# Kernel optimization log

Measured on AMD Instinct MI355X. Metric: run time of the kernel, lower is better.

Reference implementation:

```python
import jax, jax.numpy as jnp
import numpy as np

DIM = 128
HEADS = 4
HEAD_DIM = DIM // HEADS
WIN = 7
DIL = 1
EPS = 1e-5
HIDDEN = 4 * DIM  # mlp_ratio = 4.0
PAD = DIL * (WIN // 2)


def setup_inputs() -> dict:
    key = jax.random.key(0)
    ks = jax.random.split(key, 16)
    s = 0.02
    return {
        "x": jax.random.normal(ks[0], (8, DIM, 256, 256), dtype=jnp.float32),
        "n1_w": jnp.ones((DIM,), jnp.float32),
        "n1_b": jnp.zeros((DIM,), jnp.float32),
        "qkv_w": jax.random.normal(ks[1], (3 * DIM, DIM), jnp.float32) * s,
        "qkv_b": jnp.zeros((3 * DIM,), jnp.float32),
        "proj_w": jax.random.normal(ks[2], (DIM, DIM), jnp.float32) * s,
        "proj_b": jnp.zeros((DIM,), jnp.float32),
        "n2_w": jnp.ones((DIM,), jnp.float32),
        "n2_b": jnp.zeros((DIM,), jnp.float32),
        "mlp_w1": jax.random.normal(ks[3], (HIDDEN, DIM), jnp.float32) * s,
        "mlp_b1": jnp.zeros((HIDDEN,), jnp.float32),
        "mlp_w2": jax.random.normal(ks[4], (DIM, HIDDEN), jnp.float32) * s,
        "mlp_b2": jnp.zeros((DIM,), jnp.float32),
    }


def _channel_ln(x, w, b):
    # LayerNorm over channel axis (axis=1) of NCHW, per spatial location
    mu = jnp.mean(x, axis=1, keepdims=True)
    var = jnp.mean(jnp.square(x - mu), axis=1, keepdims=True)
    xn = (x - mu) * jax.lax.rsqrt(var + EPS)
    return xn * w[None, :, None, None] + b[None, :, None, None]


def _local_attn(x, qkv_w, qkv_b, proj_w, proj_b):
    B, C, H, W = x.shape
    qkv = jnp.einsum("oc,bchw->bohw", qkv_w, x) + qkv_b[None, :, None, None]
    q, k, v = jnp.split(qkv, 3, axis=1)
    q = q.reshape(B, HEADS, HEAD_DIM, H, W) * (HEAD_DIM ** -0.5)
    k = k.reshape(B, HEADS, HEAD_DIM, H, W)
    v = v.reshape(B, HEADS, HEAD_DIM, H, W)
    # boundary_pad='zeros': pad key/value maps with zeros
    pad = [(0, 0), (0, 0), (0, 0), (PAD, PAD), (PAD, PAD)]
    kp = jnp.pad(k, pad)
    vp = jnp.pad(v, pad)
    offsets = [(oi, oj) for oi in range(WIN) for oj in range(WIN)]
    scores = []
    for oi, oj in offsets:  # fixed small window loop (49 iters)
        ks = kp[..., oi * DIL : oi * DIL + H, oj * DIL : oj * DIL + W]
        scores.append(jnp.einsum("bhcij,bhcij->bhij", q, ks))
    scores = jnp.stack(scores, axis=-1)
    attn = jax.nn.softmax(scores, axis=-1)
    out = jnp.zeros_like(v)
    for idx, (oi, oj) in enumerate(offsets):
        vs = vp[..., oi * DIL : oi * DIL + H, oj * DIL : oj * DIL + W]
        out = out + attn[..., idx][:, :, None] * vs
    out = out.reshape(B, C, H, W)
    return jnp.einsum("oc,bchw->bohw", proj_w, out) + proj_b[None, :, None, None]


def _mlp(x, w1, b1, w2, b2):
    h = jnp.einsum("oc,bchw->bohw", w1, x) + b1[None, :, None, None]
    h = jax.nn.gelu(h)
    return jnp.einsum("oc,bchw->bohw", w2, h) + b2[None, :, None, None]


def reference(x, n1_w, n1_b, qkv_w, qkv_b, proj_w, proj_b, n2_w, n2_b, mlp_w1, mlp_b1, mlp_w2, mlp_b2):
    x = x + _local_attn(_channel_ln(x, n1_w, n1_b), qkv_w, qkv_b, proj_w, proj_b)
    x = x + _mlp(_channel_ln(x, n2_w, n2_b), mlp_w1, mlp_b1, mlp_w2, mlp_b2)
    return x
```

## Files before the change

### kernel.cpp

```cpp
#include <hip/hip_runtime.h>
#include <hip/hip_bf16.h>

typedef unsigned short u16;
typedef unsigned int u32;
typedef __attribute__((ext_vector_type(4))) u32 u32x4;
typedef __attribute__((ext_vector_type(2))) u32 u32x2;
typedef __attribute__((ext_vector_type(8))) __bf16 bf16x8;
typedef __attribute__((ext_vector_type(4))) float f32x4;
typedef __attribute__((ext_vector_type(4))) short short4v;

#define HW 65536

__device__ __forceinline__ u16 f2bf(float f){
  union { u32 i; float f; } v; v.f = f;
  u32 r = v.i + 0x7fffu + ((v.i >> 16) & 1u);
  return (u16)(r >> 16);
}
__device__ __forceinline__ u32 pkbf(float a, float b){
  __bf16 lo = (__bf16)a, hi = (__bf16)b;
  u16 ulo = __builtin_bit_cast(u16, lo);
  u16 uhi = __builtin_bit_cast(u16, hi);
  return (u32)ulo | ((u32)uhi << 16);
}
__device__ __forceinline__ float rcpf(float x){
#if __has_builtin(__builtin_amdgcn_rcpf)
  return __builtin_amdgcn_rcpf(x);
#else
  return 1.0f / x;
#endif
}
__device__ __forceinline__ float gelu_tanh(float v){
  float t = v * v;
  float u = fmaf(0.044715f * t, v, v);
  float z = 1.5957691216057308f * u;
  float e = __expf(-z);
  return v * rcpf(1.0f + e);
}

__device__ __forceinline__ f32x4 mfma16bf16(short4v a, short4v b, f32x4 c){
#if __has_builtin(__builtin_amdgcn_mfma_f32_16x16x16bf16_1k)
  return __builtin_amdgcn_mfma_f32_16x16x16bf16_1k(a, b, c, 0, 0, 0);
#else
  f32x4 d;
  asm volatile("v_mfma_f32_16x16x16_bf16 %0, %1, %2, %3"
               : "=v"(d) : "v"(a), "v"(b), "v"(c));
  return d;
#endif
}

__global__ __launch_bounds__(256) void k_pack(
    const float* __restrict__ qkvw, const float* __restrict__ projw,
    const float* __restrict__ w1, const float* __restrict__ w2,
    u16* __restrict__ wf)
{
  int tile = blockIdx.x;
  int t = threadIdx.x;
  int l = t >> 1, half = t & 1;
  if (l >= 64) return;
  int lg = l >> 4;
  if (tile >= 256){
    int ti = tile - 256;
    int hp = ti >> 3, m = ti & 7;
    int row = m * 16 + (l & 15);
    u16 o[4];
    #pragma unroll
    for (int j = 0; j < 4; ++j){
      int s = half * 4 + j;
      int kloc = (s < 4) ? (4 * lg + s) : (16 + 4 * lg + (s - 4));
      o[j] = f2bf(w2[(size_t)row * 512 + hp * 32 + kloc]);
    }
    u32x2 v; v[0] = (u32)o[0] | ((u32)o[1] << 16); v[1] = (u32)o[2] | ((u32)o[3] << 16);
    *(u32x2*)(wf + 131072 + ti * 512 + l * 8 + half * 4) = v;
    return;
  }
  const float* W; int base, ti;
  if (tile < 96)       { W = qkvw; base = 0;     ti = tile; }
  else if (tile < 128) { W = projw; base = 49152; ti = tile - 96; }
  else                 { W = w1;   base = 65536; ti = tile - 128; }
  int mt = ti / 4, kt = ti % 4;
  int r0 = half * 4;
  int m = mt * 16 + (l & 15);
  int kb = kt * 32 + 8 * lg + r0;
  u16 o[4];
  #pragma unroll
  for (int j = 0; j < 4; ++j) o[j] = f2bf(W[(size_t)m * 128 + kb + j]);
  u32x2 v; v[0] = (u32)o[0] | ((u32)o[1] << 16); v[1] = (u32)o[2] | ((u32)o[3] << 16);
  *(u32x2*)(wf + base + ti * 512 + l * 8 + r0) = v;
}

__global__ __launch_bounds__(256, 2) void k_ln_qkv(
    const float* __restrict__ x, const float* __restrict__ n1w,
    const float* __restrict__ n1b, const u16* __restrict__ wfq,
    const float* __restrict__ qkvb, u16* __restrict__ qkvp)
{
  __shared__ __align__(16) char smem[66560];
  float* red  = (float*)(smem + 16384);
  float* mu_s = (float*)(smem + 18432);
  float* rs_s = (float*)(smem + 18688);

  const int t = threadIdx.x;
  const int w = t >> 6, l = t & 63;
  const int P0 = blockIdx.x * 64;
  const int b = P0 >> 16;
  const int pix0 = P0 & 65535;
  const float* xb = x + ((size_t)b * 128) * HW + pix0 + l;

  float xv[32];
  float s = 0.f, s2 = 0.f;
  #pragma unroll
  for (int j = 0; j < 32; ++j){
    float v = xb[(size_t)(w * 32 + j) * HW];
    xv[j] = v; s += v; s2 += v * v;
  }
  red[w * 64 + l] = s;
  red[256 + w * 64 + l] = s2;
  __syncthreads();
  if (t < 64){
    float ss  = red[t] + red[64 + t] + red[128 + t] + red[192 + t];
    float ss2 = red[256 + t] + red[320 + t] + red[384 + t] + red[448 + t];
    float mu = ss * 0.0078125f;
    float var = ss2 * 0.0078125f - mu * mu;
    mu_s[t] = mu; rs_s[t] = rsqrtf(var + 1e-5f);
  }
  __syncthreads();
  {
    float mu = mu_s[l], rs = rs_s[l];
    #pragma unroll
    for (int jj = 0; jj < 4; ++jj){
      int c0 = w * 32 + jj * 8;
      u32x4 pk;
      #pragma unroll
      for (int k2 = 0; k2 < 4; ++k2){
        float v0 = (xv[jj*8 + k2*2    ] - mu) * rs * n1w[c0 + k2*2    ] + n1b[c0 + k2*2    ];
        float v1 = (xv[jj*8 + k2*2 + 1] - mu) * rs * n1w[c0 + k2*2 + 1] + n1b[c0 + k2*2 + 1];
        pk[k2] = pkbf(v0, v1);
      }
      *(u32x4*)(smem + l * 256 + (((w * 4 + jj) ^ (l & 7)) << 4)) = pk;
    }
  }
  __syncthreads();

  const int lg = l >> 4, ln = l & 15;
  const bf16x8* wfrag = (const bf16x8*)wfq;
  f32x4 acc[6][4];
  #pragma unroll
  for (int m = 0; m < 6; ++m)
    #pragma unroll
    for (int n = 0; n < 4; ++n) acc[m][n] = (f32x4)(0.f);
  #pragma unroll
  for (int kt = 0; kt < 4; ++kt){
    bf16x8 a[6], bb[4];
    #pragma unroll
    for (int m = 0; m < 6; ++m) a[m] = wfrag[((w*6 + m)*4 + kt)*64 + l];
    #pragma unroll
    for (int n = 0; n < 4; ++n){
      int p = n * 16 + ln;
      bb[n] = *(const bf16x8*)(smem + p * 256 + ((((kt*4 + lg)) ^ (p & 7)) << 4));
    }
    #pragma unroll
    for (int m = 0; m < 6; ++m)
      #pragma unroll
      for (int n = 0; n < 4; ++n)
        acc[m][n] = __builtin_amdgcn_mfma_f32_16x16x32_bf16(a[m], bb[n], acc[m][n], 0, 0, 0);
  }
  #pragma unroll
  for (int m = 0; m < 6; ++m)
    #pragma unroll
    for (int n = 0; n < 4; ++n){
      int o0 = w * 96 + m * 16 + 4 * lg;
      float qs = (o0 < 128) ? 0.17677669529663687f : 1.0f;
      int p = n * 16 + ln;
      u32x2 v;
      v[0] = pkbf((acc[m][n][0] + qkvb[o0+0]) * qs, (acc[m][n][1] + qkvb[o0+1]) * qs);
      v[1] = pkbf((acc[m][n][2] + qkvb[o0+2]) * qs, (acc[m][n][3] + qkvb[o0+3]) * qs);
      *(u32x2*)(smem + 16384 + p * 784 + o0 * 2) = v;
    }
  __syncthreads();
  for (int i = t; i < 3072; i += 256){
    int p = i / 48, c8 = i - p * 48;
    u32x4 v = *(const u32x4*)(smem + 16384 + p * 784 + c8 * 16);
    int sel = c8 >> 4, hh = (c8 >> 2) & 3, c0 = (c8 & 3) * 8;
    u16* plane = qkvp + (size_t)sel * 67108864ull;
    *(u32x4*)(plane + (((size_t)(b*4 + hh)) * 65536 + pix0 + p) * 32 + c0) = v;
  }
}

__global__ __launch_bounds__(256, 2) void k_attn(
    u16* qbuf, const u16* __restrict__ kbuf, const u16* __restrict__ vbuf)
{
  __shared__ __align__(16) u16 Klds[4 * 512 * 8];
  __shared__ __align__(16) u16 VT[32 * 532 + 16];
  const int t = threadIdx.x;
  const int blk = blockIdx.x;
  const int tx16 = blk & 15, ty16 = (blk >> 4) & 15;
  const int h = (blk >> 8) & 3, b = blk >> 10;
  const int y0 = ty16 * 16, x0 = tx16 * 16;
  const int bh = b * 4 + h;
  const u16* kg = kbuf + (size_t)bh * 65536 * 32;
  const u16* vg = vbuf + (size_t)bh * 65536 * 32;

  for (int i = t; i < 2130; i += 256) ((u32x4*)VT)[i] = (u32x4){0u,0u,0u,0u};
  __syncthreads();

  for (int pix = t; pix < 484; pix += 256){
    int yy = pix / 22, xx = pix - yy * 22;
    int gy = y0 + yy - 3, gx = x0 + xx - 3;
    bool ok = (gy >= 0 && gy < 256 && gx >= 0 && gx < 256);
    u32x4 kv[4], vv[4];
    #pragma unroll
    for (int j = 0; j < 4; ++j){ kv[j] = (u32x4){0u,0u,0u,0u}; vv[j] = (u32x4){0u,0u,0u,0u}; }
    if (ok){
      size_t gb = ((size_t)(gy * 256 + gx)) * 32;
      #pragma unroll
      for (int j = 0; j < 4; ++j){
        kv[j] = *(const u32x4*)(kg + gb + j * 8);
        vv[j] = *(const u32x4*)(vg + gb + j * 8);
      }
    }
    #pragma unroll
    for (int j = 0; j < 4; ++j)
      *(u32x4*)(Klds + (j * 512 + pix) * 8) = kv[j];
    int vb = yy * 24 + xx;
    #pragma unroll
    for (int j = 0; j < 4; ++j)
      #pragma unroll
      for (int ww = 0; ww < 4; ++ww){
        int c = j * 8 + ww * 2;
        VT[(c    ) * 532 + vb] = (u16)(vv[j][ww] & 0xffffu);
        VT[(c + 1) * 532 + vb] = (u16)(vv[j][ww] >> 16);
      }
  }
  __syncthreads();

  const int l = t & 63, w = t >> 6;
  const int ln = l & 15, g = l >> 4;

  bool mk[2][4];
  #pragma unroll
  for (int sl = 0; sl < 2; ++sl)
    #pragma unroll
    for (int r = 0; r < 4; ++r)
      mk[sl][r] = ((unsigned)(sl * 16 + g * 4 + r - ln)) <= 6u;

  for (int rt = 0; rt < 4; ++rt){
    int yl = rt * 4 + w;
    int qpix = (y0 + yl) * 256 + x0 + ln;
    u16* qp = qbuf + ((size_t)bh * 65536 + qpix) * 32;
    bf16x8 qf = *(const bf16x8*)(qp + g * 8);

    f32x4 S[7][2];
    #pragma unroll
    for (int oi = 0; oi < 7; ++oi){
      int rowb = (yl + oi) * 22;
      #pragma unroll
      for (int sl = 0; sl < 2; ++sl){
        bf16x8 kf = *(const bf16x8*)(Klds + (g * 512 + rowb + sl * 16 + ln) * 8);
        f32x4 z = (f32x4)(0.f);
        S[oi][sl] = __builtin_amdgcn_mfma_f32_16x16x32_bf16(kf, qf, z, 0, 0, 0);
      }
    }
    float m = -3e38f;
    #pragma unroll
    for (int oi = 0; oi < 7; ++oi)
      #pragma unroll
      for (int sl = 0; sl < 2; ++sl)
        #pragma unroll
        for (int r = 0; r < 4; ++r){
          float v = mk[sl][r] ? S[oi][sl][r] : -3e38f;
          S[oi][sl][r] = v;
          m = fmaxf(m, v);
        }
    m = fmaxf(m, __shfl_xor(m, 16));
    m = fmaxf(m, __shfl_xor(m, 32));
    float sum = 0.f;
    #pragma unroll
    for (int oi = 0; oi < 7; ++oi)
      #pragma unroll
      for (int sl = 0; sl < 2; ++sl)
        #pragma unroll
        for (int r = 0; r < 4; ++r){
          float e = __expf(S[oi][sl][r] - m);
          S[oi][sl][r] = e;
          sum += e;
        }
    sum += __shfl_xor(sum, 16);
    sum += __shfl_xor(sum, 32);
    float inv = 1.f / sum;

    short4v P[7][2];
    #pragma unroll
    for (int oi = 0; oi < 7; ++oi)
      #pragma unroll
      for (int sl = 0; sl < 2; ++sl){
        union { u32x2 u; short4v s; } cv;
        cv.u[0] = pkbf(S[oi][sl][0], S[oi][sl][1]);
        cv.u[1] = pkbf(S[oi][sl][2], S[oi][sl][3]);
        P[oi][sl] = cv.s;
      }

    f32x4 O0 = (f32x4)(0.f), O1 = (f32x4)(0.f);
    #pragma unroll
    for (int oi = 0; oi < 7; ++oi){
      int rowE = (yl + oi) * 24;
      #pragma unroll
      for (int sl = 0; sl < 2; ++sl){
        int xb = rowE + sl * 16 + 4 * g;
        short4v v0 = *(const short4v*)(VT + (ln     ) * 532 + xb);
        short4v v1 = *(const short4v*)(VT + (ln + 16) * 532 + xb);
        O0 = mfma16bf16(v0, P[oi][sl], O0);
        O1 = mfma16bf16(v1, P[oi][sl], O1);
      }
    }
    u32x2 o0, o1;
    o0[0] = pkbf(O0[0]*inv, O0[1]*inv);
    o0[1] = pkbf(O0[2]*inv, O0[3]*inv);
    o1[0] = pkbf(O1[0]*inv, O1[1]*inv);
    o1[1] = pkbf(O1[2]*inv, O1[3]*inv);
    *(u32x2*)(qp + 4 * g)      = o0;
    *(u32x2*)(qp + 16 + 4 * g) = o1;
  }
}

__global__ __launch_bounds__(256, 2) void k_proj_mlp(
    const u16* __restrict__ ao, const u16* __restrict__ wfp,
    const float* __restrict__ projb, const float* __restrict__ x,
    const float* __restrict__ n2w, const float* __restrict__ n2b,
    const u16* __restrict__ wf1, const float* __restrict__ b1,
    const u16* __restrict__ wf2, const float* __restrict__ b2,
    float* __restrict__ yout)
{
  __shared__ __align__(16) char smem[81920];
  const int t = threadIdx.x;
  const int w = t >> 6, l = t & 63, lg = l >> 4, ln = l & 15;
  const int P0 = blockIdx.x * 64;
  const int b = P0 >> 16;
  const int pix0 = P0 & 65535;

  auto stage16k = [&](const u16* gsrc, int ldsoff){
    const char* g = (const char*)gsrc;
    int base = w * 4096;
    #pragma unroll
    for (int i = 0; i < 4; ++i){
      int off = base + i * 1024;
      __builtin_amdgcn_global_load_lds(
        (const __attribute__((address_space(1))) u32*)(g + off + l * 16),
        (__attribute__((address_space(3))) u32*)(smem + ldsoff + off),
        16, 0, 0);
    }
  };

  stage16k(wfp, 16384);
  stage16k(wfp + 8192, 16384 + 16384);
  {
    int p4 = t >> 2, c4 = t & 3;
    #pragma unroll
    for (int hh = 0; hh < 4; ++hh){
      int ch = hh * 4 + c4;
      u32x4 v = *(const u32x4*)(ao + (((size_t)(b*4 + hh)) * 65536 + pix0 + p4) * 32 + c4 * 8);
      *(u32x4*)(smem + p4 * 256 + ((ch ^ (p4 & 7)) << 4)) = v;
    }
  }
  __syncthreads();

  const int p = w * 16 + ln;
  const int pixg = pix0 + p;

  bf16x8 bb[4];
  #pragma unroll
  for (int kt = 0; kt < 4; ++kt)
    bb[kt] = *(const bf16x8*)(smem + p * 256 + (((kt*4 + lg) ^ (p & 7)) << 4));

  stage16k(wf1, 49152);
  stage16k(wf2, 49152 + 16384);

  float xr[8][4];
  #pragma unroll
  for (int m = 0; m < 8; ++m){
    int c0 = m * 16 + 4 * lg;
    size_t base = ((size_t)(b * 128 + c0)) * HW + pixg;
    #pragma unroll
    for (int r = 0; r < 4; ++r) xr[m][r] = x[base + (size_t)r * HW];
  }

  f32x4 yv[8];
  #pragma unroll
  for (int m = 0; m < 8; ++m) yv[m] = (f32x4)(0.f);
  #pragma unroll
  for (int kt = 0; kt < 4; ++kt)
    #pragma unroll
    for (int m = 0; m < 8; ++m){
      bf16x8 a = *(const bf16x8*)(smem + 16384 + ((m*4 + kt) << 10) + l * 16);
      yv[m] = __builtin_amdgcn_mfma_f32_16x16x32_bf16(a, bb[kt], yv[m], 0, 0, 0);
    }

  float s = 0.f, s2 = 0.f;
  #pragma unroll
  for (int m = 0; m < 8; ++m){
    int c0 = m * 16 + 4 * lg;
    f32x4 pbv = *(const f32x4*)(projb + c0);
    #pragma unroll
    for (int r = 0; r < 4; ++r){
      float val = xr[m][r] + yv[m][r] + pbv[r];
      yv[m][r] = val;
      s += val; s2 = fmaf(val, val, s2);
    }
  }
  s  += __shfl_xor(s, 16);  s  += __shfl_xor(s, 32);
  s2 += __shfl_xor(s2, 16); s2 += __shfl_xor(s2, 32);
  float mu = s * 0.0078125f;
  float rs = rsqrtf(s2 * 0.0078125f - mu * mu + 1e-5f);

  #pragma unroll
  for (int m = 0; m < 8; ++m){
    int c0 = m * 16 + 4 * lg;
    f32x4 wv = *(const f32x4*)(n2w + c0);
    f32x4 bv = *(const f32x4*)(n2b + c0);
    float x0 = (yv[m][0] - mu) * rs * wv[0] + bv[0];
    float x1 = (yv[m][1] - mu) * rs * wv[1] + bv[1];
    float x2 = (yv[m][2] - mu) * rs * wv[2] + bv[2];
    float x3 = (yv[m][3] - mu) * rs * wv[3] + bv[3];
    int g8 = c0 >> 3;
    u32x2 pk; pk[0] = pkbf(x0, x1); pk[1] = pkbf(x2, x3);
    *(u32x2*)(smem + p * 256 + ((g8 ^ (p & 7)) << 4) + ((lg & 1) << 3)) = pk;
  }
  #pragma unroll
  for (int kt = 0; kt < 4; ++kt)
    bb[kt] = *(const bf16x8*)(smem + p * 256 + (((kt*4 + lg) ^ (p & 7)) << 4));

  __syncthreads();

  f32x4 acc2[8];
  #pragma unroll
  for (int m = 0; m < 8; ++m) acc2[m] = (f32x4)(0.f);

  for (int c = 0; c < 8; ++c){
    const int cur = (c + 1) & 1;
    const int curoff = 16384 + (cur << 15);
    if (c < 7){
      const int nxtoff = 16384 + ((cur ^ 1) << 15);
      stage16k(wf1 + (c + 1) * 8192, nxtoff);
      stage16k(wf2 + (c + 1) * 8192, nxtoff + 16384);
    }
    f32x4 h0a = (f32x4)(0.f), h0b = (f32x4)(0.f);
    f32x4 h1a = (f32x4)(0.f), h1b = (f32x4)(0.f);
    #pragma unroll
    for (int kt = 0; kt < 4; ++kt){
      bf16x8 a0 = *(const bf16x8*)(smem + curoff + ((0*4 + kt) << 10) + l * 16);
      bf16x8 a1 = *(const bf16x8*)(smem + curoff + ((1*4 + kt) << 10) + l * 16);
      bf16x8 a2 = *(const bf16x8*)(smem + curoff + ((2*4 + kt) << 10) + l * 16);
      bf16x8 a3 = *(const bf16x8*)(smem + curoff + ((3*4 + kt) << 10) + l * 16);
      h0a = __builtin_amdgcn_mfma_f32_16x16x32_bf16(a0, bb[kt], h0a, 0, 0, 0);
      h0b = __builtin_amdgcn_mfma_f32_16x16x32_bf16(a1, bb[kt], h0b, 0, 0, 0);
      h1a = __builtin_amdgcn_mfma_f32_16x16x32_bf16(a2, bb[kt], h1a, 0, 0, 0);
      h1b = __builtin_amdgcn_mfma_f32_16x16x32_bf16(a3, bb[kt], h1b, 0, 0, 0);
    }
    bf16x8 hf0, hf1;
    {
      int hp0 = 2 * c;
      f32x4 b1a = *(const f32x4*)(b1 + hp0 * 32 + 4 * lg);
      f32x4 b1b = *(const f32x4*)(b1 + hp0 * 32 + 16 + 4 * lg);
      union { u32x4 u; bf16x8 h; } hf;
      hf.u[0] = pkbf(gelu_tanh(h0a[0] + b1a[0]), gelu_tanh(h0a[1] + b1a[1]));
      hf.u[1] = pkbf(gelu_tanh(h0a[2] + b1a[2]), gelu_tanh(h0a[3] + b1a[3]));
      hf.u[2] = pkbf(gelu_tanh(h0b[0] + b1b[0]), gelu_tanh(h0b[1] + b1b[1]));
      hf.u[3] = pkbf(gelu_tanh(h0b[2] + b1b[2]), gelu_tanh(h0b[3] + b1b[3]));
      hf0 = hf.h;
      int hp1 = 2 * c + 1;
      f32x4 c1a = *(const f32x4*)(b1 + hp1 * 32 + 4 * lg);
      f32x4 c1b = *(const f32x4*)(b1 + hp1 * 32 + 16 + 4 * lg);
      hf.u[0] = pkbf(gelu_tanh(h1a[0] + c1a[0]), gelu_tanh(h1a[1] + c1a[1]));
      hf.u[1] = pkbf(gelu_tanh(h1a[2] + c1a[2]), gelu_tanh(h1a[3] + c1a[3]));
      hf.u[2] = pkbf(gelu_tanh(h1b[0] + c1b[0]), gelu_tanh(h1b[1] + c1b[1]));
      hf.u[3] = pkbf(gelu_tanh(h1b[2] + c1b[2]), gelu_tanh(h1b[3] + c1b[3]));
      hf1 = hf.h;
    }
    #pragma unroll
    for (int m = 0; m < 8; ++m){
      bf16x8 a0 = *(const bf16x8*)(smem + curoff + 16384 + ((0*8 + m) << 10) + l * 16);
      acc2[m] = __builtin_amdgcn_mfma_f32_16x16x32_bf16(a0, hf0, acc2[m], 0, 0, 0);
      bf16x8 a1 = *(const bf16x8*)(smem + curoff + 16384 + ((1*8 + m) << 10) + l * 16);
      acc2[m] = __builtin_amdgcn_mfma_f32_16x16x32_bf16(a1, hf1, acc2[m], 0, 0, 0);
    }
    if (c < 7) __syncthreads();
  }

  #pragma unroll
  for (int m = 0; m < 8; ++m){
    int c0 = m * 16 + 4 * lg;
    f32x4 b2v = *(const f32x4*)(b2 + c0);
    size_t base = ((size_t)(b * 128 + c0)) * HW + pixg;
    #pragma unroll
    for (int r = 0; r < 4; ++r)
      yout[base + (size_t)r * HW] = yv[m][r] + acc2[m][r] + b2v[r];
  }
}

extern "C" void kernel_launch(void* const* d_in, const int* in_sizes, int n_in,
                              void* d_out, int out_size, void* d_ws, size_t ws_size,
                              hipStream_t stream)
{
  const float* x    = (const float*)d_in[0];
  const float* n1w  = (const float*)d_in[1];
  const float* n1b  = (const float*)d_in[2];
  const float* qkvw = (const float*)d_in[3];
  const float* qkvb = (const float*)d_in[4];
  const float* pw   = (const float*)d_in[5];
  const float* pb   = (const float*)d_in[6];
  const float* n2w  = (const float*)d_in[7];
  const float* n2b  = (const float*)d_in[8];
  const float* w1   = (const float*)d_in[9];
  const float* b1   = (const float*)d_in[10];
  const float* w2   = (const float*)d_in[11];
  const float* b2   = (const float*)d_in[12];

  u16* qkvp = (u16*)d_ws;
  u16* qbuf = qkvp;
  u16* kbuf = qkvp + 67108864ull;
  u16* vbuf = qkvp + 134217728ull;
  u16* wf   = qkvp + 201326592ull;
  u16* wfq = wf;
  u16* wfp = wf + 49152;
  u16* wf1 = wf + 65536;
  u16* wf2 = wf + 131072;
  float* y = (float*)d_out;

  k_pack<<<384, 256, 0, stream>>>(qkvw, pw, w1, w2, wf);
  k_ln_qkv<<<8192, 256, 0, stream>>>(x, n1w, n1b, wfq, qkvb, qkvp);
  k_attn<<<8192, 256, 0, stream>>>(qbuf, kbuf, vbuf);
  k_proj_mlp<<<8192, 256, 0, stream>>>(qbuf, wfp, pb, x, n2w, n2b, wf1, b1, wf2, b2, y);
}
```

Measured before the change: 733.7 us.

## Process 128 pixels per block in proj+MLP kernel to reuse weight fragments

The fused proj/LN2/MLP kernel now handles 128 pixels per block instead of 64, with each wave computing two 16-pixel column tiles that share every LDS weight fragment load. LDS is cut from 80 KB to 64 KB by reusing the activation region for the MLP weight double buffer after the projection GEMM, at the cost of an extra barrier. The grid is halved. The aim is to halve weight-staging traffic and LDS reads per MFMA, in exchange for higher register pressure that may spill or lower occupancy.

```diff
diff --git a/kernel.cpp b/kernel.cpp
--- a/kernel.cpp
+++ b/kernel.cpp
@@ -10,6 +10,7 @@
 typedef __attribute__((ext_vector_type(4))) short short4v;
 
 #define HW 65536
+#define MFMA32(a, b, c) __builtin_amdgcn_mfma_f32_16x16x32_bf16((a), (b), (c), 0, 0, 0)
 
 __device__ __forceinline__ u16 f2bf(float f){
   union { u32 i; float f; } v; v.f = f;
@@ -161,7 +162,7 @@
     for (int m = 0; m < 6; ++m)
       #pragma unroll
       for (int n = 0; n < 4; ++n)
-        acc[m][n] = __builtin_amdgcn_mfma_f32_16x16x32_bf16(a[m], bb[n], acc[m][n], 0, 0, 0);
+        acc[m][n] = MFMA32(a[m], bb[n], acc[m][n]);
   }
   #pragma unroll
   for (int m = 0; m < 6; ++m)
@@ -256,7 +257,7 @@
       for (int sl = 0; sl < 2; ++sl){
         bf16x8 kf = *(const bf16x8*)(Klds + (g * 512 + rowb + sl * 16 + ln) * 8);
         f32x4 z = (f32x4)(0.f);
-        S[oi][sl] = __builtin_amdgcn_mfma_f32_16x16x32_bf16(kf, qf, z, 0, 0, 0);
+        S[oi][sl] = MFMA32(kf, qf, z);
       }
     }
     float m = -3e38f;
@@ -329,10 +330,10 @@
     const u16* __restrict__ wf2, const float* __restrict__ b2,
     float* __restrict__ yout)
 {
-  __shared__ __align__(16) char smem[81920];
+  __shared__ __align__(16) char smem[65536];
   const int t = threadIdx.x;
   const int w = t >> 6, l = t & 63, lg = l >> 4, ln = l & 15;
-  const int P0 = blockIdx.x * 64;
+  const int P0 = blockIdx.x * 128;
   const int b = P0 >> 16;
   const int pix0 = P0 & 65535;
 
@@ -349,10 +350,11 @@
     }
   };
 
-  stage16k(wfp, 16384);
-  stage16k(wfp + 8192, 16384 + 16384);
-  {
-    int p4 = t >> 2, c4 = t & 3;
+  stage16k(wfp, 32768);
+  stage16k(wfp + 8192, 49152);
+  #pragma unroll
+  for (int half = 0; half < 2; ++half){
+    int p4 = half * 64 + (t >> 2), c4 = t & 3;
     #pragma unroll
     for (int hh = 0; hh < 4; ++hh){
       int ch = hh * 4 + c4;
@@ -362,125 +364,134 @@
   }
   __syncthreads();
 
-  const int p = w * 16 + ln;
-  const int pixg = pix0 + p;
-
-  bf16x8 bb[4];
+  const int pA = w * 32 + ln;
+  const int pB = pA + 16;
+
+  bf16x8 bbA[4], bbB[4];
+  #pragma unroll
+  for (int kt = 0; kt < 4; ++kt){
+    bbA[kt] = *(const bf16x8*)(smem + pA * 256 + (((kt*4 + lg) ^ (pA & 7)) << 4));
+    bbB[kt] = *(const bf16x8*)(smem + pB * 256 + (((kt*4 + lg) ^ (pB & 7)) << 4));
+  }
+
+  f32x4 yvA[8], yvB[8];
+  #pragma unroll
+  for (int m = 0; m < 8; ++m){ yvA[m] = (f32x4)(0.f); yvB[m] = (f32x4)(0.f); }
   #pragma unroll
   for (int kt = 0; kt < 4; ++kt)
-    bb[kt] = *(const bf16x8*)(smem + p * 256 + (((kt*4 + lg) ^ (p & 7)) << 4));
-
-  stage16k(wf1, 49152);
-  stage16k(wf2, 49152 + 16384);
-
-  float xr[8][4];
-  #pragma unroll
-  for (int m = 0; m < 8; ++m){
-    int c0 = m * 16 + 4 * lg;
-    size_t base = ((size_t)(b * 128 + c0)) * HW + pixg;
-    #pragma unroll
-    for (int r = 0; r < 4; ++r) xr[m][r] = x[base + (size_t)r * HW];
-  }
-
-  f32x4 yv[8];
-  #pragma unroll
-  for (int m = 0; m < 8; ++m) yv[m] = (f32x4)(0.f);
-  #pragma unroll
-  for (int kt = 0; kt < 4; ++kt)
     #pragma unroll
     for (int m = 0; m < 8; ++m){
-      bf16x8 a = *(const bf16x8*)(smem + 16384 + ((m*4 + kt) << 10) + l * 16);
-      yv[m] = __builtin_amdgcn_mfma_f32_16x16x32_bf16(a, bb[kt], yv[m], 0, 0, 0);
-    }
-
-  float s = 0.f, s2 = 0.f;
+      bf16x8 a = *(const bf16x8*)(smem + 32768 + ((m*4 + kt) << 10) + l * 16);
+      yvA[m] = MFMA32(a, bbA[kt], yvA[m]);
+      yvB[m] = MFMA32(a, bbB[kt], yvB[m]);
+    }
+  __syncthreads();
+  stage16k(wf1, 32768);
+  stage16k(wf2, 49152);
+
+  float sA = 0.f, s2A = 0.f, sB = 0.f, s2B = 0.f;
   #pragma unroll
   for (int m = 0; m < 8; ++m){
     int c0 = m * 16 + 4 * lg;
     f32x4 pbv = *(const f32x4*)(projb + c0);
+    size_t baseA = ((size_t)(b * 128 + c0)) * HW + pix0 + pA;
     #pragma unroll
     for (int r = 0; r < 4; ++r){
-      float val = xr[m][r] + yv[m][r] + pbv[r];
-      yv[m][r] = val;
-      s += val; s2 = fmaf(val, val, s2);
-    }
-  }
-  s  += __shfl_xor(s, 16);  s  += __shfl_xor(s, 32);
-  s2 += __shfl_xor(s2, 16); s2 += __shfl_xor(s2, 32);
-  float mu = s * 0.0078125f;
-  float rs = rsqrtf(s2 * 0.0078125f - mu * mu + 1e-5f);
+      float vA = x[baseA + (size_t)r * HW] + yvA[m][r] + pbv[r];
+      float vB = x[baseA + 16 + (size_t)r * HW] + yvB[m][r] + pbv[r];
+      yvA[m][r] = vA; yvB[m][r] = vB;
+      sA += vA; s2A = fmaf(vA, vA, s2A);
+      sB += vB; s2B = fmaf(vB, vB, s2B);
+    }
+  }
+  sA  += __shfl_xor(sA, 16);  sA  += __shfl_xor(sA, 32);
+  s2A += __shfl_xor(s2A, 16); s2A += __shfl_xor(s2A, 32);
+  sB  += __shfl_xor(sB, 16);  sB  += __shfl_xor(sB, 32);
+  s2B += __shfl_xor(s2B, 16); s2B += __shfl_xor(s2B, 32);
+  float muA = sA * 0.0078125f;
+  float rsA = rsqrtf(s2A * 0.0078125f - muA * muA + 1e-5f);
+  float muB = sB * 0.0078125f;
+  float rsB = rsqrtf(s2B * 0.0078125f - muB * muB + 1e-5f);
 
   #pragma unroll
   for (int m = 0; m < 8; ++m){
     int c0 = m * 16 + 4 * lg;
     f32x4 wv = *(const f32x4*)(n2w + c0);
     f32x4 bv = *(const f32x4*)(n2b + c0);
-    float x0 = (yv[m][0] - mu) * rs * wv[0] + bv[0];
-    float x1 = (yv[m][1] - mu) * rs * wv[1] + bv[1];
-    float x2 = (yv[m][2] - mu) * rs * wv[2] + bv[2];
-    float x3 = (yv[m][3] - mu) * rs * wv[3] + bv[3];
     int g8 = c0 >> 3;
-    u32x2 pk; pk[0] = pkbf(x0, x1); pk[1] = pkbf(x2, x3);
-    *(u32x2*)(smem + p * 256 + ((g8 ^ (p & 7)) << 4) + ((lg & 1) << 3)) = pk;
-  }
-  #pragma unroll
-  for (int kt = 0; kt < 4; ++kt)
-    bb[kt] = *(const bf16x8*)(smem + p * 256 + (((kt*4 + lg) ^ (p & 7)) << 4));
-
-  __syncthreads();
-
-  f32x4 acc2[8];
-  #pragma unroll
-  for (int m = 0; m < 8; ++m) acc2[m] = (f32x4)(0.f);
+    u32x2 pkA, pkB;
+    pkA[0] = pkbf((yvA[m][0]-muA)*rsA*wv[0]+bv[0], (yvA[m][1]-muA)*rsA*wv[1]+bv[1]);
+    pkA[1] = pkbf((yvA[m][2]-muA)*rsA*wv[2]+bv[2], (yvA[m][3]-muA)*rsA*wv[3]+bv[3]);
+    pkB[0] = pkbf((yvB[m][0]-muB)*rsB*wv[0]+bv[0], (yvB[m][1]-muB)*rsB*wv[1]+bv[1]);
+    pkB[1] = pkbf((yvB[m][2]-muB)*rsB*wv[2]+bv[2], (yvB[m][3]-muB)*rsB*wv[3]+bv[3]);
+    *(u32x2*)(smem + pA * 256 + ((g8 ^ (pA & 7)) << 4) + ((lg & 1) << 3)) = pkA;
+    *(u32x2*)(smem + pB * 256 + ((g8 ^ (pB & 7)) << 4) + ((lg & 1) << 3)) = pkB;
+  }
+  #pragma unroll
+  for (int kt = 0; kt < 4; ++kt){
+    bbA[kt] = *(const bf16x8*)(smem + pA * 256 + (((kt*4 + lg) ^ (pA & 7)) << 4));
+    bbB[kt] = *(const bf16x8*)(smem + pB * 256 + (((kt*4 + lg) ^ (pB & 7)) << 4));
+  }
+  __syncthreads();
+
+  f32x4 acA[8], acB[8];
+  #pragma unroll
+  for (int m = 0; m < 8; ++m){ acA[m] = (f32x4)(0.f); acB[m] = (f32x4)(0.f); }
 
   for (int c = 0; c < 8; ++c){
-    const int cur = (c + 1) & 1;
-    const int curoff = 16384 + (cur << 15);
+    const int curoff = (c & 1) ? 0 : 32768;
     if (c < 7){
-      const int nxtoff = 16384 + ((cur ^ 1) << 15);
-      stage16k(wf1 + (c + 1) * 8192, nxtoff);
-      stage16k(wf2 + (c + 1) * 8192, nxtoff + 16384);
-    }
-    f32x4 h0a = (f32x4)(0.f), h0b = (f32x4)(0.f);
-    f32x4 h1a = (f32x4)(0.f), h1b = (f32x4)(0.f);
-    #pragma unroll
-    for (int kt = 0; kt < 4; ++kt){
-      bf16x8 a0 = *(const bf16x8*)(smem + curoff + ((0*4 + kt) << 10) + l * 16);
-      bf16x8 a1 = *(const bf16x8*)(smem + curoff + ((1*4 + kt) << 10) + l * 16);
-      bf16x8 a2 = *(const bf16x8*)(smem + curoff + ((2*4 + kt) << 10) + l * 16);
-      bf16x8 a3 = *(const bf16x8*)(smem + curoff + ((3*4 + kt) << 10) + l * 16);
-      h0a = __builtin_amdgcn_mfma_f32_16x16x32_bf16(a0, bb[kt], h0a, 0, 0, 0);
-      h0b = __builtin_amdgcn_mfma_f32_16x16x32_bf16(a1, bb[kt], h0b, 0, 0, 0);
-      h1a = __builtin_amdgcn_mfma_f32_16x16x32_bf16(a2, bb[kt], h1a, 0, 0, 0);
-      h1b = __builtin_amdgcn_mfma_f32_16x16x32_bf16(a3, bb[kt], h1b, 0, 0, 0);
-    }
-    bf16x8 hf0, hf1;
+      const int nxt = curoff ^ 32768;
+      stage16k(wf1 + (c + 1) * 8192, nxt);
+      stage16k(wf2 + (c + 1) * 8192, nxt + 16384);
+    }
+    f32x4 hA[4], hB[4];
+    #pragma unroll
+    for (int mt = 0; mt < 4; ++mt){ hA[mt] = (f32x4)(0.f); hB[mt] = (f32x4)(0.f); }
+    #pragma unroll
+    for (int kt = 0; kt < 4; ++kt)
+      #pragma unroll
+      for (int mt = 0; mt < 4; ++mt){
+        bf16x8 a = *(const bf16x8*)(smem + curoff + ((mt*4 + kt) << 10) + l * 16);
+        hA[mt] = MFMA32(a, bbA[kt], hA[mt]);
+        hB[mt] = MFMA32(a, bbB[kt], hB[mt]);
+      }
+    int hb0 = c * 64 + 4 * lg;
+    f32x4 b1v[4];
+    #pragma unroll
+    for (int mt = 0; mt < 4; ++mt) b1v[mt] = *(const f32x4*)(b1 + hb0 + mt * 16);
+    bf16x8 hfA0, hfA1, hfB0, hfB1;
     {
-      int hp0 = 2 * c;
-      f32x4 b1a = *(const f32x4*)(b1 + hp0 * 32 + 4 * lg);
-      f32x4 b1b = *(const f32x4*)(b1 + hp0 * 32 + 16 + 4 * lg);
-      union { u32x4 u; bf16x8 h; } hf;
-      hf.u[0] = pkbf(gelu_tanh(h0a[0] + b1a[0]), gelu_tanh(h0a[1] + b1a[1]));
-      hf.u[1] = pkbf(gelu_tanh(h0a[2] + b1a[2]), gelu_tanh(h0a[3] + b1a[3]));
-      hf.u[2] = pkbf(gelu_tanh(h0b[0] + b1b[0]), gelu_tanh(h0b[1] + b1b[1]));
-      hf.u[3] = pkbf(gelu_tanh(h0b[2] + b1b[2]), gelu_tanh(h0b[3] + b1b[3]));
-      hf0 = hf.h;
-      int hp1 = 2 * c + 1;
-      f32x4 c1a = *(const f32x4*)(b1 + hp1 * 32 + 4 * lg);
-      f32x4 c1b = *(const f32x4*)(b1 + hp1 * 32 + 16 + 4 * lg);
-      hf.u[0] = pkbf(gelu_tanh(h1a[0] + c1a[0]), gelu_tanh(h1a[1] + c1a[1]));
-      hf.u[1] = pkbf(gelu_tanh(h1a[2] + c1a[2]), gelu_tanh(h1a[3] + c1a[3]));
-      hf.u[2] = pkbf(gelu_tanh(h1b[0] + c1b[0]), gelu_tanh(h1b[1] + c1b[1]));
-      hf.u[3] = pkbf(gelu_tanh(h1b[2] + c1b[2]), gelu_tanh(h1b[3] + c1b[3]));
-      hf1 = hf.h;
-    }
-    #pragma unroll
-    for (int m = 0; m < 8; ++m){
-      bf16x8 a0 = *(const bf16x8*)(smem + curoff + 16384 + ((0*8 + m) << 10) + l * 16);
-      acc2[m] = __builtin_amdgcn_mfma_f32_16x16x32_bf16(a0, hf0, acc2[m], 0, 0, 0);
-      bf16x8 a1 = *(const bf16x8*)(smem + curoff + 16384 + ((1*8 + m) << 10) + l * 16);
-      acc2[m] = __builtin_amdgcn_mfma_f32_16x16x32_bf16(a1, hf1, acc2[m], 0, 0, 0);
-    }
+      union { u32x4 u; bf16x8 h; } uu;
+      uu.u[0] = pkbf(gelu_tanh(hA[0][0]+b1v[0][0]), gelu_tanh(hA[0][1]+b1v[0][1]));
+      uu.u[1] = pkbf(gelu_tanh(hA[0][2]+b1v[0][2]), gelu_tanh(hA[0][3]+b1v[0][3]));
+      uu.u[2] = pkbf(gelu_tanh(hA[1][0]+b1v[1][0]), gelu_tanh(hA[1][1]+b1v[1][1]));
+      uu.u[3] = pkbf(gelu_tanh(hA[1][2]+b1v[1][2]), gelu_tanh(hA[1][3]+b1v[1][3]));
+      hfA0 = uu.h;
+      uu.u[0] = pkbf(gelu_tanh(hA[2][0]+b1v[2][0]), gelu_tanh(hA[2][1]+b1v[2][1]));
+      uu.u[1] = pkbf(gelu_tanh(hA[2][2]+b1v[2][2]), gelu_tanh(hA[2][3]+b1v[2][3]));
+      uu.u[2] = pkbf(gelu_tanh(hA[3][0]+b1v[3][0]), gelu_tanh(hA[3][1]+b1v[3][1]));
+      uu.u[3] = pkbf(gelu_tanh(hA[3][2]+b1v[3][2]), gelu_tanh(hA[3][3]+b1v[3][3]));
+      hfA1 = uu.h;
+      uu.u[0] = pkbf(gelu_tanh(hB[0][0]+b1v[0][0]), gelu_tanh(hB[0][1]+b1v[0][1]));
+      uu.u[1] = pkbf(gelu_tanh(hB[0][2]+b1v[0][2]), gelu_tanh(hB[0][3]+b1v[0][3]));
+      uu.u[2] = pkbf(gelu_tanh(hB[1][0]+b1v[1][0]), gelu_tanh(hB[1][1]+b1v[1][1]));
+      uu.u[3] = pkbf(gelu_tanh(hB[1][2]+b1v[1][2]), gelu_tanh(hB[1][3]+b1v[1][3]));
+      hfB0 = uu.h;
+      uu.u[0] = pkbf(gelu_tanh(hB[2][0]+b1v[2][0]), gelu_tanh(hB[2][1]+b1v[2][1]));
+      uu.u[1] = pkbf(gelu_tanh(hB[2][2]+b1v[2][2]), gelu_tanh(hB[2][3]+b1v[2][3]));
+      uu.u[2] = pkbf(gelu_tanh(hB[3][0]+b1v[3][0]), gelu_tanh(hB[3][1]+b1v[3][1]));
+      uu.u[3] = pkbf(gelu_tanh(hB[3][2]+b1v[3][2]), gelu_tanh(hB[3][3]+b1v[3][3]));
+      hfB1 = uu.h;
+    }
+    #pragma unroll
+    for (int hpl = 0; hpl < 2; ++hpl)
+      #pragma unroll
+      for (int m = 0; m < 8; ++m){
+        bf16x8 a = *(const bf16x8*)(smem + curoff + 16384 + ((hpl*8 + m) << 10) + l * 16);
+        acA[m] = MFMA32(a, hpl ? hfA1 : hfA0, acA[m]);
+        acB[m] = MFMA32(a, hpl ? hfB1 : hfB0, acB[m]);
+      }
     if (c < 7) __syncthreads();
   }
 
@@ -488,10 +499,12 @@
   for (int m = 0; m < 8; ++m){
     int c0 = m * 16 + 4 * lg;
     f32x4 b2v = *(const f32x4*)(b2 + c0);
-    size_t base = ((size_t)(b * 128 + c0)) * HW + pixg;
-    #pragma unroll
-    for (int r = 0; r < 4; ++r)
-      yout[base + (size_t)r * HW] = yv[m][r] + acc2[m][r] + b2v[r];
+    size_t baseA = ((size_t)(b * 128 + c0)) * HW + pix0 + pA;
+    #pragma unroll
+    for (int r = 0; r < 4; ++r){
+      yout[baseA + (size_t)r * HW]      = yvA[m][r] + acA[m][r] + b2v[r];
+      yout[baseA + 16 + (size_t)r * HW] = yvB[m][r] + acB[m][r] + b2v[r];
+    }
   }
 }
 
@@ -527,5 +540,5 @@
   k_pack<<<384, 256, 0, stream>>>(qkvw, pw, w1, w2, wf);
   k_ln_qkv<<<8192, 256, 0, stream>>>(x, n1w, n1b, wfq, qkvb, qkvp);
   k_attn<<<8192, 256, 0, stream>>>(qbuf, kbuf, vbuf);
-  k_proj_mlp<<<8192, 256, 0, stream>>>(qbuf, wfp, pb, x, n2w, n2b, wf1, b1, wf2, b2, y);
-}
+  k_proj_mlp<<<4096, 256, 0, stream>>>(qbuf, wfp, pb, x, n2w, n2b, wf1, b1, wf2, b2, y);
+}
```

Measured after the change: 685.4 us. 1.07x faster.
